# Kernel tuning notes

Measured on AMD Instinct MI355X. Metric: run time of the kernel, lower is better.

## Reference

```python
import jax, jax.numpy as jnp
import numpy as np

# frontier sizes per layer (input -> output) and edges per block
N = [400000, 120000, 20000, 4000]
E = [1800000, 200000, 20000]
IN_FEATS, N_HIDDEN, N_CLASSES = 128, 256, 47


def setup_inputs() -> dict:
    key = jax.random.key(0)
    ks = jax.random.split(key, 16)
    inp = {}
    inp["x"] = jax.random.normal(ks[0], (N[0], IN_FEATS), dtype=jnp.float32)
    # block edge lists: src in [0, N[l]), dst in [0, N[l+1))
    for l in range(3):
        inp[f"src{l}"] = jax.random.randint(ks[1 + 2 * l], (E[l],), 0, N[l], dtype=jnp.int32)
        inp[f"dst{l}"] = jax.random.randint(ks[2 + 2 * l], (E[l],), 0, N[l + 1], dtype=jnp.int32)
    dims = [(IN_FEATS, N_HIDDEN), (N_HIDDEN, N_HIDDEN), (N_HIDDEN, N_CLASSES)]
    for l, (din, dout) in enumerate(dims):
        scale = 1.0 / np.sqrt(din)
        inp[f"Ws{l}"] = jax.random.normal(ks[7 + 3 * l], (din, dout), dtype=jnp.float32) * scale
        inp[f"Wn{l}"] = jax.random.normal(ks[8 + 3 * l], (din, dout), dtype=jnp.float32) * scale
        inp[f"b{l}"] = jnp.zeros((dout,), dtype=jnp.float32)
    return inp


def sage_layer(h, src, dst, n_dst, Ws, Wn, b):
    # mean aggregation over incoming edges (gather -> segment-reduce)
    msgs = h[src]  # [E, din]
    neigh_sum = jax.ops.segment_sum(msgs, dst, num_segments=n_dst)
    deg = jax.ops.segment_sum(jnp.ones((dst.shape[0], 1), h.dtype), dst, num_segments=n_dst)
    neigh_mean = neigh_sum / jnp.maximum(deg, 1.0)
    # DGL block convention: dst nodes are the first n_dst src nodes
    return h[:n_dst] @ Ws + neigh_mean @ Wn + b


def reference(x, src0, dst0, src1, dst1, src2, dst2,
              Ws0, Wn0, b0, Ws1, Wn1, b1, Ws2, Wn2, b2):
    h = jax.nn.relu(sage_layer(x, src0, dst0, N[1], Ws0, Wn0, b0))
    h = jax.nn.relu(sage_layer(h, src1, dst1, N[2], Ws1, Wn1, b1))
    h = sage_layer(h, src2, dst2, N[3], Ws2, Wn2, b2)
    return h
```

## Files before the change

### kernel.cpp

```cpp
#include <hip/hip_runtime.h>
#include <hip/hip_bf16.h>

typedef __hip_bfloat16 bf16;
typedef __attribute__((ext_vector_type(8))) short short8;
typedef __attribute__((ext_vector_type(4))) float float4v;

#define N1 120000
#define N2 20000
#define N3 4000
#define E0 1800000
#define E1 200000
#define E2 20000
#define D_IN 128
#define D_HID 256
#define D_OUT 47

__device__ __forceinline__ void stv(float* p, float v) { *p = v; }
__device__ __forceinline__ void stv(bf16* p, float v) { *p = __float2bfloat16(v); }

__device__ __forceinline__ unsigned short f2bu(float v) {
    union { bf16 h; unsigned short u; } c;
    c.h = __float2bfloat16(v);
    return c.u;
}
__device__ __forceinline__ short f2bs(float v) { return (short)f2bu(v); }
__device__ __forceinline__ float bu2f(unsigned short u) { return __uint_as_float(((unsigned)u) << 16); }

__device__ __forceinline__ short8 load8(const bf16* p) {
    union { uint4 u; short8 s; } r;
    r.u = *(const uint4*)p;
    return r.s;
}
__device__ __forceinline__ short8 load8(const float* p) {
    float4 a = *(const float4*)p;
    float4 b = *(const float4*)(p + 4);
    short8 s;
    s[0] = f2bs(a.x); s[1] = f2bs(a.y); s[2] = f2bs(a.z); s[3] = f2bs(a.w);
    s[4] = f2bs(b.x); s[5] = f2bs(b.y); s[6] = f2bs(b.z); s[7] = f2bs(b.w);
    return s;
}

__global__ __launch_bounds__(256) void convert_x(const float* __restrict__ x,
                                                 bf16* __restrict__ xb, int n8) {
    int i = blockIdx.x * blockDim.x + threadIdx.x;
    if (i >= n8) return;
    const float* p = x + (size_t)i * 8;
    float4 a = *(const float4*)p;
    float4 b = *(const float4*)(p + 4);
    union { uint4 u; short s[8]; } o;
    o.s[0] = f2bs(a.x); o.s[1] = f2bs(a.y); o.s[2] = f2bs(a.z); o.s[3] = f2bs(a.w);
    o.s[4] = f2bs(b.x); o.s[5] = f2bs(b.y); o.s[6] = f2bs(b.z); o.s[7] = f2bs(b.w);
    *(uint4*)(xb + (size_t)i * 8) = o.u;
}

__global__ void wt_batch(const float* W0s, const float* W0n, const float* W1s,
                         const float* W1n, const float* W2s, const float* W2n,
                         bf16* T0s, bf16* T0n, bf16* T1s, bf16* T1n, bf16* T2s, bf16* T2n) {
    int i = blockIdx.x * blockDim.x + threadIdx.x;
    const float* W; bf16* T; int K, N, j;
    if      (i <  32768) { W = W0s; T = T0s; K = 128; N = 256; j = i; }
    else if (i <  65536) { W = W0n; T = T0n; K = 128; N = 256; j = i - 32768; }
    else if (i < 131072) { W = W1s; T = T1s; K = 256; N = 256; j = i - 65536; }
    else if (i < 196608) { W = W1n; T = T1n; K = 256; N = 256; j = i - 131072; }
    else if (i < 208896) { W = W2s; T = T2s; K = 256; N = 47;  j = i - 196608; }
    else if (i < 221184) { W = W2n; T = T2n; K = 256; N = 47;  j = i - 208896; }
    else return;
    int n = j / K, k = j - n * K;
    float v = (n < N) ? W[(size_t)k * N + n] : 0.f;
    T[j] = __float2bfloat16(v);
}

__global__ void hist_batch(const int* __restrict__ d0, const int* __restrict__ d1,
                           const int* __restrict__ d2, int* __restrict__ c0,
                           int* __restrict__ c1, int* __restrict__ c2) {
    int i = blockIdx.x * blockDim.x + threadIdx.x;
    if (i < E0) atomicAdd(&c0[d0[i]], 1);
    else if (i < E0 + E1) atomicAdd(&c1[d1[i - E0]], 1);
    else if (i < E0 + E1 + E2) atomicAdd(&c2[d2[i - E0 - E1]], 1);
}

__global__ __launch_bounds__(256) void scan_chunk_batch(
    const int* __restrict__ c0, const int* __restrict__ c1, const int* __restrict__ c2,
    int* __restrict__ r0, int* __restrict__ r1, int* __restrict__ r2, int* __restrict__ bsum) {
    __shared__ int sd[256];
    int b = blockIdx.x, t = threadIdx.x;
    const int* cnt; int* out; int* bs; int n, cb;
    if (b < 118)      { cnt = c0; out = r0; bs = bsum;       n = N1; cb = b; }
    else if (b < 138) { cnt = c1; out = r1; bs = bsum + 128; n = N2; cb = b - 118; }
    else              { cnt = c2; out = r2; bs = bsum + 256; n = N3; cb = b - 138; }
    int base = cb * 1024 + t * 4;
    int v[4]; int s = 0;
    #pragma unroll
    for (int j = 0; j < 4; j++) { int i = base + j; v[j] = (i < n) ? cnt[i] : 0; s += v[j]; }
    sd[t] = s;
    __syncthreads();
    for (int off = 1; off < 256; off <<= 1) {
        int x = (t >= off) ? sd[t - off] : 0;
        __syncthreads();
        sd[t] += x;
        __syncthreads();
    }
    int run = sd[t] - s;
    #pragma unroll
    for (int j = 0; j < 4; j++) { int i = base + j; if (i < n) out[i] = run; run += v[j]; }
    if (t == 255) bs[cb] = sd[255];
}

__global__ __launch_bounds__(256) void scan_bsum_batch(int* __restrict__ bsum,
        int* __restrict__ r0, int* __restrict__ r1, int* __restrict__ r2) {
    __shared__ int sd[256];
    int l = blockIdx.x, t = threadIdx.x;
    int B = (l == 0) ? 118 : (l == 1 ? 20 : 4);
    int* bs = bsum + l * 128;
    int s = (t < B) ? bs[t] : 0;
    sd[t] = s;
    __syncthreads();
    for (int off = 1; off < 256; off <<= 1) {
        int x = (t >= off) ? sd[t - off] : 0;
        __syncthreads();
        sd[t] += x;
        __syncthreads();
    }
    if (t < B) bs[t] = sd[t] - s;
    if (t == 255) {
        if (l == 0) r0[N1] = sd[255];
        else if (l == 1) r1[N2] = sd[255];
        else r2[N3] = sd[255];
    }
}

__global__ void scan_add_batch(int* __restrict__ r0, int* __restrict__ r1,
                               int* __restrict__ r2, const int* __restrict__ bsum) {
    int i = blockIdx.x * blockDim.x + threadIdx.x;
    if (i < N1) r0[i] += bsum[i >> 10];
    else if (i < N1 + N2) { int j = i - N1; r1[j] += bsum[128 + (j >> 10)]; }
    else if (i < N1 + N2 + N3) { int j = i - N1 - N2; r2[j] += bsum[256 + (j >> 10)]; }
}

__global__ void csr_fill_batch(const int* __restrict__ s0, const int* __restrict__ d0,
                               const int* __restrict__ s1, const int* __restrict__ d1,
                               const int* __restrict__ s2, const int* __restrict__ d2,
                               int* __restrict__ c0, int* __restrict__ c1, int* __restrict__ c2,
                               const int* __restrict__ r0, const int* __restrict__ r1,
                               const int* __restrict__ r2, int* __restrict__ col0,
                               int* __restrict__ col1, int* __restrict__ col2) {
    int i = blockIdx.x * blockDim.x + threadIdx.x;
    if (i < E0) {
        int d = d0[i];
        col0[r0[d] + atomicSub(&c0[d], 1) - 1] = s0[i];
    } else if (i < E0 + E1) {
        int e = i - E0; int d = d1[e];
        col1[r1[d] + atomicSub(&c1[d], 1) - 1] = s1[e];
    } else if (i < E0 + E1 + E2) {
        int e = i - E0 - E1; int d = d2[e];
        col2[r2[d] + atomicSub(&c2[d], 1) - 1] = s2[e];
    }
}

template <int DIN, typename T>
__global__ __launch_bounds__(256) void gather_mean(const T* __restrict__ h,
        const int* __restrict__ rp, const int* __restrict__ col,
        int n_dst, bf16* __restrict__ agg) {
    int gw = (blockIdx.x * blockDim.x + threadIdx.x) >> 6;
    int lane = threadIdx.x & 63;
    if (gw >= n_dst) return;
    int beg = rp[gw], end = rp[gw + 1];
    constexpr int VP = DIN / 64;
    float s[VP] = {};

    auto accum = [&](int srcn) {
        const T* hp = h + (size_t)srcn * DIN + lane * VP;
        if constexpr (sizeof(T) == 4) {
            float2 v = *(const float2*)hp;
            s[0] += v.x; s[1] += v.y;
        } else if constexpr (VP == 2) {
            union { unsigned u; unsigned short us[2]; } r;
            r.u = *(const unsigned*)hp;
            s[0] += bu2f(r.us[0]); s[1] += bu2f(r.us[1]);
        } else {
            union { uint2 u; unsigned short us[4]; } r;
            r.u = *(const uint2*)hp;
            #pragma unroll
            for (int j = 0; j < 4; j++) s[j] += bu2f(r.us[j]);
        }
    };

    int e = beg;
    for (; e + 3 < end; e += 4) {
        int a0 = col[e], a1 = col[e + 1], a2 = col[e + 2], a3 = col[e + 3];
        accum(a0); accum(a1); accum(a2); accum(a3);
    }
    for (; e < end; ++e) accum(col[e]);

    float inv = 1.f / fmaxf((float)(end - beg), 1.f);
    #pragma unroll
    for (int j = 0; j < VP; j++) s[j] *= inv;

    bf16* ap = agg + (size_t)gw * DIN + lane * VP;
    if constexpr (VP == 2) {
        ushort2 o; o.x = f2bu(s[0]); o.y = f2bu(s[1]);
        *(ushort2*)ap = o;
    } else {
        ushort4 o; o.x = f2bu(s[0]); o.y = f2bu(s[1]); o.z = f2bu(s[2]); o.w = f2bu(s[3]);
        *(ushort4*)ap = o;
    }
}

template <int DIN>
__global__ __launch_bounds__(256) void gather_mean_w(const bf16* __restrict__ h,
        const int* __restrict__ rp, const int* __restrict__ col,
        int n_dst, bf16* __restrict__ agg) {
    constexpr int G = DIN / 8;
    constexpr int R = 64 / G;
    int gw = (blockIdx.x * blockDim.x + threadIdx.x) >> 6;
    int lane = threadIdx.x & 63;
    if (gw >= n_dst) return;
    int beg = rp[gw], end = rp[gw + 1];
    int g = lane / G;
    int p = lane & (G - 1);

    float s[8] = {};

    auto accum = [&](const short8& v) {
        #pragma unroll
        for (int j = 0; j < 8; j++) s[j] += bu2f((unsigned short)v[j]);
    };

    int e = beg;
    for (; e + 2 * R <= end; e += 2 * R) {
        int sa = col[e + g];
        int sb = col[e + R + g];
        short8 va = load8(h + (size_t)sa * DIN + p * 8);
        short8 vb = load8(h + (size_t)sb * DIN + p * 8);
        accum(va); accum(vb);
    }
    for (; e + R <= end; e += R) {
        int sa = col[e + g];
        short8 va = load8(h + (size_t)sa * DIN + p * 8);
        accum(va);
    }
    if (e < end) {
        bool act = (e + g) < end;
        int sa = col[act ? (e + g) : beg];
        short8 va = load8(h + (size_t)sa * DIN + p * 8);
        if (act) accum(va);
    }

    #pragma unroll
    for (int m = G; m < 64; m <<= 1) {
        #pragma unroll
        for (int j = 0; j < 8; j++) s[j] += __shfl_xor(s[j], m, 64);
    }

    float inv = 1.f / fmaxf((float)(end - beg), 1.f);
    if (g == 0) {
        union { uint4 u; unsigned short us[8]; } o;
        #pragma unroll
        for (int j = 0; j < 8; j++) o.us[j] = f2bu(s[j] * inv);
        *(uint4*)(agg + (size_t)gw * DIN + p * 8) = o.u;
    }
}

template <typename TA, typename TC, bool RELU>
__global__ __launch_bounds__(256) void gemm_mfma(
    const TA* __restrict__ A, const bf16* __restrict__ Mn,
    const bf16* __restrict__ Wst, const bf16* __restrict__ Wnt,
    const float* __restrict__ bias, TC* __restrict__ C,
    int M, int Nstore, int Npad, int K) {
    __shared__ short As[128][48];
    __shared__ short Bs[128][48];

    int tid = threadIdx.x;
    int m0 = blockIdx.x * 128;
    int n0 = blockIdx.y * 128;
    int lane = tid & 63, wid = tid >> 6;
    int wm = (wid & 1) * 64, wn = (wid >> 1) * 64;
    int l15 = lane & 15, quad = lane >> 4;

    float4v acc[4][4] = {};

    int nsteps = (2 * K) >> 5;
    int r = tid >> 2, c = (tid & 3) << 3;
    for (int s = 0; s < nsteps; ++s) {
        int ks = s << 5;
        bool self = ks < K;
        int ko = self ? ks : ks - K;
        #pragma unroll
        for (int it = 0; it < 2; ++it) {
            int rr = r + it * 64;
            {
                int gm = m0 + rr;
                short8 v = (short8)0;
                if (gm < M) {
                    if (self) v = load8(A  + (size_t)gm * K + ko + c);
                    else      v = load8(Mn + (size_t)gm * K + ko + c);
                }
                *(short8*)&As[rr][c] = v;
            }
            {
                int gn = n0 + rr;
                short8 w = (short8)0;
                if (gn < Npad) {
                    const bf16* Wp = self ? Wst : Wnt;
                    w = load8(Wp + (size_t)gn * K + ko + c);
                }
                *(short8*)&Bs[rr][c] = w;
            }
        }
        __syncthreads();
        short8 af[4], bfr[4];
        #pragma unroll
        for (int i = 0; i < 4; ++i)
            af[i] = *(const short8*)&As[wm + i * 16 + l15][quad * 8];
        #pragma unroll
        for (int j = 0; j < 4; ++j)
            bfr[j] = *(const short8*)&Bs[wn + j * 16 + l15][quad * 8];
        #pragma unroll
        for (int i = 0; i < 4; ++i)
            #pragma unroll
            for (int j = 0; j < 4; ++j)
                acc[i][j] = __builtin_amdgcn_mfma_f32_16x16x32_bf16(af[i], bfr[j], acc[i][j], 0, 0, 0);
        __syncthreads();
    }

    #pragma unroll
    for (int i = 0; i < 4; ++i) {
        #pragma unroll
        for (int j = 0; j < 4; ++j) {
            int gn = n0 + wn + j * 16 + l15;
            if (gn >= Nstore) continue;
            float bv = bias[gn];
            #pragma unroll
            for (int rr = 0; rr < 4; ++rr) {
                int gm = m0 + wm + i * 16 + quad * 4 + rr;
                if (gm >= M) continue;
                float v = acc[i][j][rr] + bv;
                if (RELU) v = fmaxf(v, 0.f);
                stv(&C[(size_t)gm * Nstore + gn], v);
            }
        }
    }
}

extern "C" void kernel_launch(void* const* d_in, const int* in_sizes, int n_in,
                              void* d_out, int out_size, void* d_ws, size_t ws_size,
                              hipStream_t stream) {
    const float* x    = (const float*)d_in[0];
    const int*  src0 = (const int*)d_in[1];
    const int*  dst0 = (const int*)d_in[2];
    const int*  src1 = (const int*)d_in[3];
    const int*  dst1 = (const int*)d_in[4];
    const int*  src2 = (const int*)d_in[5];
    const int*  dst2 = (const int*)d_in[6];
    const float* Ws0 = (const float*)d_in[7];
    const float* Wn0 = (const float*)d_in[8];
    const float* b0  = (const float*)d_in[9];
    const float* Ws1 = (const float*)d_in[10];
    const float* Wn1 = (const float*)d_in[11];
    const float* b1  = (const float*)d_in[12];
    const float* Ws2 = (const float*)d_in[13];
    const float* Wn2 = (const float*)d_in[14];
    const float* b2  = (const float*)d_in[15];
    float* out = (float*)d_out;

    char* W = (char*)d_ws;
    int* cnt0  = (int*)(W + 0);
    int* cnt1  = (int*)(W + 480000);
    int* cnt2  = (int*)(W + 560000);
    int* rp0   = (int*)(W + 576000);
    int* rp1   = (int*)(W + 1056004);
    int* rp2   = (int*)(W + 1136008);
    int* col0  = (int*)(W + 1152016);
    int* col1  = (int*)(W + 8352016);
    int* col2  = (int*)(W + 9152016);
    int* bsum  = (int*)(W + 9232016);
    bf16* Wst0 = (bf16*)(W + 9233552);
    bf16* Wnt0 = (bf16*)(W + 9299088);
    bf16* Wst1 = (bf16*)(W + 9364624);
    bf16* Wnt1 = (bf16*)(W + 9495696);
    bf16* Wst2 = (bf16*)(W + 9626768);
    bf16* Wnt2 = (bf16*)(W + 9651344);

    const size_t BASE = 9676032;
    const bool use_xb = ws_size >= (size_t)205000000;
    bf16* xb = (bf16*)(W + BASE);
    size_t agg0_off = BASE + (use_xb ? 102400000 : 0);
    bf16* agg0 = (bf16*)(W + agg0_off);
    bf16* h1   = (bf16*)(W + agg0_off + 30720000);
    bf16* agg1 = (bf16*)(W + BASE);
    bf16* h2   = (bf16*)(W + BASE + 10240000);
    bf16* agg2 = (bf16*)(W + BASE + 20480000);

    hipMemsetAsync(W, 0, 576000, stream);
    if (use_xb) {
        int n8 = 400000 * D_IN / 8;
        convert_x<<<(n8 + 255) / 256, 256, 0, stream>>>(x, xb, n8);
    }
    wt_batch<<<(221184 + 255) / 256, 256, 0, stream>>>(Ws0, Wn0, Ws1, Wn1, Ws2, Wn2,
                                                       Wst0, Wnt0, Wst1, Wnt1, Wst2, Wnt2);
    const int ETOT = E0 + E1 + E2;
    hist_batch<<<(ETOT + 255) / 256, 256, 0, stream>>>(dst0, dst1, dst2, cnt0, cnt1, cnt2);
    scan_chunk_batch<<<142, 256, 0, stream>>>(cnt0, cnt1, cnt2, rp0, rp1, rp2, bsum);
    scan_bsum_batch<<<3, 256, 0, stream>>>(bsum, rp0, rp1, rp2);
    scan_add_batch<<<(N1 + N2 + N3 + 255) / 256, 256, 0, stream>>>(rp0, rp1, rp2, bsum);
    csr_fill_batch<<<(ETOT + 255) / 256, 256, 0, stream>>>(src0, dst0, src1, dst1, src2, dst2,
                                                           cnt0, cnt1, cnt2, rp0, rp1, rp2,
                                                           col0, col1, col2);

    if (use_xb) {
        gather_mean_w<D_IN><<<(N1 + 3) / 4, 256, 0, stream>>>(xb, rp0, col0, N1, agg0);
        dim3 grid((N1 + 127) / 128, 2);
        gemm_mfma<bf16, bf16, true><<<grid, 256, 0, stream>>>(xb, agg0, Wst0, Wnt0, b0, h1, N1, 256, 256, 128);
    } else {
        gather_mean<D_IN, float><<<(N1 + 3) / 4, 256, 0, stream>>>(x, rp0, col0, N1, agg0);
        dim3 grid((N1 + 127) / 128, 2);
        gemm_mfma<float, bf16, true><<<grid, 256, 0, stream>>>(x, agg0, Wst0, Wnt0, b0, h1, N1, 256, 256, 128);
    }

    gather_mean_w<D_HID><<<(N2 + 3) / 4, 256, 0, stream>>>(h1, rp1, col1, N2, agg1);
    {
        dim3 grid((N2 + 127) / 128, 2);
        gemm_mfma<bf16, bf16, true><<<grid, 256, 0, stream>>>(h1, agg1, Wst1, Wnt1, b1, h2, N2, 256, 256, 256);
    }

    gather_mean_w<D_HID><<<(N3 + 3) / 4, 256, 0, stream>>>(h2, rp2, col2, N3, agg2);
    {
        dim3 grid((N3 + 127) / 128, 1);
        gemm_mfma<bf16, float, false><<<grid, 256, 0, stream>>>(h2, agg2, Wst2, Wnt2, b2, out, N3, 47, 48, 256);
    }
}
```

Before: 721.5 us.

## Build CSR via two-pass bucketed scatter with shared-memory local atomics

Replaces the single-pass CSR fill, which does global atomics and a scattered write per edge, with two passes. The first appends (src,dst) pairs into 128-destination buckets using per-bucket global atomic counters. The second has one block per bucket place edges into final positions using LDS atomics, aiming for more localized global writes. It adds an extra pass over packed edge pairs, extra workspace, and heavy contention on the few bucket counters. It only runs when the workspace is large enough.

```diff
diff --git a/kernel.cpp b/kernel.cpp
--- a/kernel.cpp
+++ b/kernel.cpp
@@ -14,6 +14,10 @@
 #define D_IN 128
 #define D_HID 256
 #define D_OUT 47
+
+#define NB0 938
+#define NB1 157
+#define NB2 32
 
 __device__ __forceinline__ void stv(float* p, float v) { *p = v; }
 __device__ __forceinline__ void stv(bf16* p, float v) { *p = __float2bfloat16(v); }
@@ -154,6 +158,66 @@
     } else if (i < E0 + E1 + E2) {
         int e = i - E0 - E1; int d = d2[e];
         col2[r2[d] + atomicSub(&c2[d], 1) - 1] = s2[e];
+    }
+}
+
+__global__ void csr_append_batch(const int* __restrict__ s0, const int* __restrict__ d0,
+                                 const int* __restrict__ s1, const int* __restrict__ d1,
+                                 const int* __restrict__ s2, const int* __restrict__ d2,
+                                 const int* __restrict__ r0, const int* __restrict__ r1,
+                                 const int* __restrict__ r2,
+                                 int* __restrict__ cur0, int* __restrict__ cur1,
+                                 int* __restrict__ cur2,
+                                 uint2* __restrict__ pk0, uint2* __restrict__ pk1,
+                                 uint2* __restrict__ pk2) {
+    int i = blockIdx.x * blockDim.x + threadIdx.x;
+    if (i < E0) {
+        int d = d0[i]; int b = d >> 7;
+        int base = r0[b << 7];
+        int pos = atomicAdd(&cur0[b], 1);
+        uint2 p; p.x = (unsigned)s0[i]; p.y = (unsigned)d;
+        pk0[base + pos] = p;
+    } else if (i < E0 + E1) {
+        int e = i - E0; int d = d1[e]; int b = d >> 7;
+        int base = r1[b << 7];
+        int pos = atomicAdd(&cur1[b], 1);
+        uint2 p; p.x = (unsigned)s1[e]; p.y = (unsigned)d;
+        pk1[base + pos] = p;
+    } else if (i < E0 + E1 + E2) {
+        int e = i - E0 - E1; int d = d2[e]; int b = d >> 7;
+        int base = r2[b << 7];
+        int pos = atomicAdd(&cur2[b], 1);
+        uint2 p; p.x = (unsigned)s2[e]; p.y = (unsigned)d;
+        pk2[base + pos] = p;
+    }
+}
+
+__global__ __launch_bounds__(256) void csr_bucket_fill(
+        const int* __restrict__ r0, const int* __restrict__ r1, const int* __restrict__ r2,
+        const uint2* __restrict__ pk0, const uint2* __restrict__ pk1,
+        const uint2* __restrict__ pk2,
+        int* __restrict__ col0, int* __restrict__ col1, int* __restrict__ col2) {
+    __shared__ int lofs[128];
+    int b = blockIdx.x;
+    const int* rp; const uint2* pk; int* col; int lb, n;
+    if (b < NB0)            { rp = r0; pk = pk0; col = col0; lb = b;             n = N1; }
+    else if (b < NB0 + NB1) { rp = r1; pk = pk1; col = col1; lb = b - NB0;       n = N2; }
+    else                    { rp = r2; pk = pk2; col = col2; lb = b - NB0 - NB1; n = N3; }
+    int dlo = lb << 7;
+    int dhi = min(dlo + 128, n);
+    int base = rp[dlo];
+    int cnt = rp[dhi] - base;
+    int t = threadIdx.x;
+    if (t < 128) {
+        int dd = dlo + t;
+        lofs[t] = (dd < dhi) ? (rp[dd] - base) : 0;
+    }
+    __syncthreads();
+    for (int e = t; e < cnt; e += 256) {
+        uint2 p = pk[base + e];
+        int k = (int)p.y - dlo;
+        int pos = atomicAdd(&lofs[k], 1);
+        col[base + pos] = (int)p.x;
     }
 }
 
@@ -391,7 +455,16 @@
     bf16* h2   = (bf16*)(W + BASE + 10240000);
     bf16* agg2 = (bf16*)(W + BASE + 20480000);
 
+    const bool bucketed = ws_size >= (size_t)227000000;
+    int*  cur0 = (int*)(W + 210000000);
+    int*  cur1 = (int*)(W + 210003752);
+    int*  cur2 = (int*)(W + 210004380);
+    uint2* pk0 = (uint2*)(W + 210004512);
+    uint2* pk1 = (uint2*)(W + 224404512);
+    uint2* pk2 = (uint2*)(W + 226004512);
+
     hipMemsetAsync(W, 0, 576000, stream);
+    if (bucketed) hipMemsetAsync(W + 210000000, 0, 4512, stream);
     if (use_xb) {
         int n8 = 400000 * D_IN / 8;
         convert_x<<<(n8 + 255) / 256, 256, 0, stream>>>(x, xb, n8);
@@ -403,9 +476,17 @@
     scan_chunk_batch<<<142, 256, 0, stream>>>(cnt0, cnt1, cnt2, rp0, rp1, rp2, bsum);
     scan_bsum_batch<<<3, 256, 0, stream>>>(bsum, rp0, rp1, rp2);
     scan_add_batch<<<(N1 + N2 + N3 + 255) / 256, 256, 0, stream>>>(rp0, rp1, rp2, bsum);
-    csr_fill_batch<<<(ETOT + 255) / 256, 256, 0, stream>>>(src0, dst0, src1, dst1, src2, dst2,
-                                                           cnt0, cnt1, cnt2, rp0, rp1, rp2,
-                                                           col0, col1, col2);
+    if (bucketed) {
+        csr_append_batch<<<(ETOT + 255) / 256, 256, 0, stream>>>(
+            src0, dst0, src1, dst1, src2, dst2, rp0, rp1, rp2,
+            cur0, cur1, cur2, pk0, pk1, pk2);
+        csr_bucket_fill<<<NB0 + NB1 + NB2, 256, 0, stream>>>(
+            rp0, rp1, rp2, pk0, pk1, pk2, col0, col1, col2);
+    } else {
+        csr_fill_batch<<<(ETOT + 255) / 256, 256, 0, stream>>>(src0, dst0, src1, dst1, src2, dst2,
+                                                               cnt0, cnt1, cnt2, rp0, rp1, rp2,
+                                                               col0, col1, col2);
+    }
 
     if (use_xb) {
         gather_mean_w<D_IN><<<(N1 + 3) / 4, 256, 0, stream>>>(xb, rp0, col0, N1, agg0);
```

Result: slower. 1.094 ms (+51.6%).
